# Optimization experiments

Hardware: AMD Instinct MI355X
Metric: run time of the kernel (lower is better)

Reference implementation:

```python
import jax, jax.numpy as jnp
import numpy as np

N_NODES = 50000
N_EDGES = 800000
D_IN = 128
HIDDEN = 128
NUM_GRAPHS = 64
NUM_CLASSES = 6


def setup_inputs() -> dict:
    key = jax.random.key(0)
    ks = jax.random.split(key, 12)
    x = jax.random.normal(ks[0], (N_NODES, D_IN), dtype=jnp.float32)
    edge_index = jax.random.randint(ks[1], (2, N_EDGES), 0, N_NODES, dtype=jnp.int64)
    batch = jnp.sort(jax.random.randint(ks[2], (N_NODES,), 0, NUM_GRAPHS, dtype=jnp.int64))
    def glorot(k, fan_in, fan_out):
        s = jnp.sqrt(6.0 / (fan_in + fan_out)).astype(jnp.float32)
        return jax.random.uniform(k, (fan_in, fan_out), jnp.float32, -s, s)
    W0 = glorot(ks[3], D_IN, HIDDEN)
    b0 = jnp.zeros((HIDDEN,), jnp.float32)
    W1 = glorot(ks[4], HIDDEN, HIDDEN)
    b1 = jnp.zeros((HIDDEN,), jnp.float32)
    W2 = glorot(ks[5], HIDDEN, HIDDEN)
    b2 = jnp.zeros((HIDDEN,), jnp.float32)
    lin_W = glorot(ks[6], HIDDEN, NUM_CLASSES)
    lin_b = jnp.zeros((NUM_CLASSES,), jnp.float32)
    return {"x": x, "edge_index": edge_index, "batch": batch,
            "W0": W0, "b0": b0, "W1": W1, "b1": b1, "W2": W2, "b2": b2,
            "lin_W": lin_W, "lin_b": lin_b}


def reference(x, edge_index, batch, W0, b0, W1, b1, W2, b2, lin_W, lin_b):
    # GCNConv (PyG default): add self-loops, symmetric degree norm,
    # out = scatter_add(norm * (xW)[src] -> dst) + bias, then ReLU.
    loop = jnp.arange(N_NODES, dtype=edge_index.dtype)
    src = jnp.concatenate([edge_index[0], loop])  # message sources (x_j)
    dst = jnp.concatenate([edge_index[1], loop])  # aggregation targets
    deg = jax.ops.segment_sum(jnp.ones_like(dst, x.dtype), dst, num_segments=N_NODES)
    dinv = jnp.where(deg > 0, jax.lax.rsqrt(deg), 0.0)
    norm = (dinv[src] * dinv[dst])[:, None]  # [E+N, 1]

    h = x
    for W, b in ((W0, b0), (W1, b1), (W2, b2)):
        hw = h @ W                                   # [N, H] dense projection
        agg = jax.ops.segment_sum(hw[src] * norm, dst, num_segments=N_NODES)
        h = jax.nn.relu(agg + b)

    # global_mean_pool over graph ids
    counts = jax.ops.segment_sum(jnp.ones((N_NODES,), x.dtype), batch, num_segments=NUM_GRAPHS)
    embedding = jax.ops.segment_sum(h, batch, num_segments=NUM_GRAPHS) / jnp.maximum(counts, 1.0)[:, None]
    # dropout is identity in eval mode
    logits = embedding @ lin_W + lin_b
    return logits, embedding
```

## Files before the change

### kernel.cpp

```cpp
#include <hip/hip_runtime.h>

#define N_NODES 50000
#define HIDDEN 128
#define NUM_GRAPHS 64
#define NUM_CLASSES 6
#define SLOT_SHIFT 6
#define NB 392
#define BUCKET_CAP 3072
#define P1_CHUNK 2048
#define CONV_BLOCKS 96
#define LSTR 136

typedef __attribute__((ext_vector_type(8))) short short8;
typedef __attribute__((ext_vector_type(4))) float float4v;
typedef __attribute__((ext_vector_type(2))) float float2v;

__device__ __forceinline__ unsigned short f2b(float f) {
    unsigned u = __float_as_uint(f);
    return (unsigned short)((u + 0x7FFFu + ((u >> 16) & 1u)) >> 16);
}
__device__ __forceinline__ unsigned char f2e4m3(float f) {
    return (unsigned char)(__builtin_amdgcn_cvt_pk_fp8_f32(f, f, 0, false) & 0xFF);
}

__global__ __launch_bounds__(512) void pass1(const float* __restrict__ W0, const float* __restrict__ W1,
                                             const float* __restrict__ W2, unsigned short* __restrict__ wb,
                                             const int* __restrict__ src, const int* __restrict__ dst,
                                             int* __restrict__ gcursor, unsigned* __restrict__ ebuf, int e) {
    if (blockIdx.x < CONV_BLOCKS) {
        int i = blockIdx.x * 512 + threadIdx.x;
        int wsel = i >> 14;
        int r = i & 16383;
        int j = r & 7;
        int lane = (r >> 3) & 63;
        int f = r >> 9;
        int ki = f >> 3, nt = f & 7;
        int k = ki * 32 + (lane >> 4) * 8 + j;
        int c = nt * 16 + (lane & 15);
        const float* W = (wsel == 0) ? W0 : ((wsel == 1) ? W1 : W2);
        wb[i] = f2b(W[k * 128 + c]);
        return;
    }
    __shared__ unsigned hist[NB];
    __shared__ unsigned base[NB];
    const int t = threadIdx.x;
    const int start = (blockIdx.x - CONV_BLOCKS) * P1_CHUNK;
    for (int i = t; i < NB; i += 512) hist[i] = 0;
    __syncthreads();
    int lb[4];
    unsigned pk[4], lr[4];
#pragma unroll
    for (int k = 0; k < 4; k++) {
        int i = start + k * 512 + t;
        lb[k] = -1;
        if (i < e) {
            int d = dst[i];
            int s = src[i];
            lb[k] = d >> 7;
            pk[k] = ((unsigned)(d & 127) << 16) | (unsigned)s;
            lr[k] = atomicAdd(&hist[lb[k]], 1u);
        }
    }
    __syncthreads();
    for (int b = t; b < NB; b += 512)
        base[b] = (unsigned)atomicAdd(&gcursor[b], (int)hist[b]);
    __syncthreads();
#pragma unroll
    for (int k = 0; k < 4; k++) {
        if (lb[k] >= 0) {
            unsigned pos = base[lb[k]] + lr[k];
            if (pos < BUCKET_CAP) ebuf[lb[k] * BUCKET_CAP + pos] = pk[k];
        }
    }
}

__global__ __launch_bounds__(512) void pass2(const unsigned* __restrict__ ebuf, const int* __restrict__ gcursor,
                                             const float* __restrict__ x,
                                             unsigned short* __restrict__ csr16, int* __restrict__ cntc,
                                             float* __restrict__ dinv, unsigned char* __restrict__ xs8, int n) {
    __shared__ unsigned short csr_lds[128 * 64];
    __shared__ unsigned cnt[128];
    const int b = blockIdx.x;
    const int t = threadIdx.x;
    if (t < 128) {
        cnt[t] = 0;
        csr_lds[t * 64] = (unsigned short)(b * 128 + t);
    }
    __syncthreads();
    const int nb = min(gcursor[b], BUCKET_CAP);
    for (int i = t; i < nb; i += 512) {
        unsigned e = ebuf[b * BUCKET_CAP + i];
        int dl = (int)(e >> 16);
        unsigned r = atomicAdd(&cnt[dl], 1u);
        if (r < 63) csr_lds[dl * 64 + 1 + r] = (unsigned short)(e & 0xFFFFu);
    }
    __syncthreads();
    {
        const unsigned* cu = (const unsigned*)csr_lds;
        unsigned* gout = (unsigned*)(csr16 + (size_t)b * 8192);
#pragma unroll
        for (int it = 0; it < 8; it++) gout[it * 512 + t] = cu[it * 512 + t];
    }
    if (t < 128) {
        int node = b * 128 + t;
        if (node < n) {
            int deg1 = (int)cnt[t] + 1;
            cntc[node] = min(deg1, 64);
            dinv[node] = rsqrtf((float)deg1);
        }
    }
#pragma unroll
    for (int it = 0; it < 8; it++) {
        int idx = it * 512 + t;
        int nl = idx >> 5;
        int el = (idx & 31) * 4;
        int gnode = b * 128 + nl;
        if (gnode < n) {
            float sc = rsqrtf((float)((int)cnt[nl] + 1));
            float4 v = *(const float4*)&x[gnode * 128 + el];
            unsigned lo = __builtin_amdgcn_cvt_pk_fp8_f32(v.x * sc, v.y * sc, 0, false);
            unsigned pkd = __builtin_amdgcn_cvt_pk_fp8_f32(v.z * sc, v.w * sc, lo, true);
            *(unsigned*)&xs8[gnode * 128 + el] = pkd;
        }
    }
}

__global__ __launch_bounds__(256) void fused_layer(const unsigned char* __restrict__ hs8,
                                                   const int* __restrict__ cntc,
                                                   const unsigned short* __restrict__ csr16,
                                                   const float* __restrict__ dinv,
                                                   const unsigned short* __restrict__ wb,
                                                   const float* __restrict__ bias,
                                                   const float* __restrict__ rowscale,
                                                   unsigned char* __restrict__ hout8,
                                                   const int* __restrict__ batchp,
                                                   float* __restrict__ embp) {
    __shared__ __align__(16) unsigned short tlds[16 * LSTR];
    __shared__ int bsh[16];
    const int wave = threadIdx.x >> 6;
    const int lane = threadIdx.x & 63;
    const int grp = lane >> 4;
    const int fl = lane & 15;
    const int node0 = blockIdx.x * 16;
    const int base_node = node0 + wave * 4;

    int nbv[4], mycv[4];
#pragma unroll
    for (int i = 0; i < 4; i++) nbv[i] = cntc[base_node + i];
#pragma unroll
    for (int i = 0; i < 4; i++)
        mycv[i] = (lane < nbv[i]) ? (int)csr16[((base_node + i) << SLOT_SHIFT) + lane] : 0;

    for (int i = 0; i < 4; i++) {
        const int node = base_node + i;
        const int nb = nbv[i];
        const int nbm1 = nb - 1;
        const int myc = mycv[i];
        float2v a01 = {0.f, 0.f}, a23 = {0.f, 0.f}, a45 = {0.f, 0.f}, a67 = {0.f, 0.f};

        const int nfull = nb >> 4;
        for (int h = 0; h < nfull; h++) {
            const int base = h << 4;
            int cc[4];
#pragma unroll
            for (int k = 0; k < 4; k++) cc[k] = __shfl(myc, base + k * 4 + grp, 64);
            uint2 u[4];
#pragma unroll
            for (int k = 0; k < 4; k++) u[k] = *(const uint2*)&hs8[cc[k] * 128 + fl * 8];
#pragma unroll
            for (int k = 0; k < 4; k++) {
                a01 += __builtin_amdgcn_cvt_pk_f32_fp8(u[k].x, false);
                a23 += __builtin_amdgcn_cvt_pk_f32_fp8(u[k].x, true);
                a45 += __builtin_amdgcn_cvt_pk_f32_fp8(u[k].y, false);
                a67 += __builtin_amdgcn_cvt_pk_f32_fp8(u[k].y, true);
            }
        }
        if (nb & 15) {
            const int base = nfull << 4;
            int cc[4];
            float mm[4];
#pragma unroll
            for (int k = 0; k < 4; k++) {
                int e = base + k * 4 + grp;
                mm[k] = (e < nb) ? 1.f : 0.f;
                cc[k] = __shfl(myc, min(e, nbm1), 64);
            }
            uint2 u[4];
#pragma unroll
            for (int k = 0; k < 4; k++) u[k] = *(const uint2*)&hs8[cc[k] * 128 + fl * 8];
#pragma unroll
            for (int k = 0; k < 4; k++) {
                float2v m2 = {mm[k], mm[k]};
                a01 += m2 * __builtin_amdgcn_cvt_pk_f32_fp8(u[k].x, false);
                a23 += m2 * __builtin_amdgcn_cvt_pk_f32_fp8(u[k].x, true);
                a45 += m2 * __builtin_amdgcn_cvt_pk_f32_fp8(u[k].y, false);
                a67 += m2 * __builtin_amdgcn_cvt_pk_f32_fp8(u[k].y, true);
            }
        }

        float acc[8] = {a01.x, a01.y, a23.x, a23.y, a45.x, a45.y, a67.x, a67.y};
#pragma unroll
        for (int j = 0; j < 8; j++) {
            acc[j] += __shfl_xor(acc[j], 16, 64);
            acc[j] += __shfl_xor(acc[j], 32, 64);
        }
        if (grp == 0) {
            const float dv = dinv[node];
            short8 o;
#pragma unroll
            for (int j = 0; j < 8; j++) o[j] = (short)f2b(acc[j] * dv);
            *(short8*)&tlds[(wave * 4 + i) * LSTR + fl * 8] = o;
        }
    }
    if (embp && threadIdx.x < 16) bsh[threadIdx.x] = batchp[node0 + threadIdx.x];
    __syncthreads();

    const int m = fl;
    const int quad = grp;
    const int nt0 = wave * 2;
    const short* B = (const short*)wb;
    float4v acc2[2];
    acc2[0] = (float4v){0.f, 0.f, 0.f, 0.f};
    acc2[1] = (float4v){0.f, 0.f, 0.f, 0.f};
#pragma unroll
    for (int ki = 0; ki < 4; ki++) {
        short8 a = *(const short8*)&tlds[m * LSTR + ki * 32 + quad * 8];
#pragma unroll
        for (int q = 0; q < 2; q++) {
            short8 b = *(const short8*)&B[((ki * 8 + nt0 + q) * 64 + lane) * 8];
            acc2[q] = __builtin_amdgcn_mfma_f32_16x16x32_bf16(a, b, acc2[q], 0, 0, 0);
        }
    }

    if (!embp) {
        float sc[4];
#pragma unroll
        for (int reg = 0; reg < 4; reg++) {
            int row = node0 + quad * 4 + reg;
            sc[reg] = rowscale[row];
        }
#pragma unroll
        for (int q = 0; q < 2; q++) {
            int c = (nt0 + q) * 16 + m;
            float bv = bias[c];
#pragma unroll
            for (int reg = 0; reg < 4; reg++) {
                int row = node0 + quad * 4 + reg;
                float v = fmaxf(acc2[q][reg] + bv, 0.f) * sc[reg];
                hout8[row * 128 + c] = f2e4m3(v);
            }
        }
    } else {
        const int g0 = bsh[0], g15 = bsh[15];
#pragma unroll
        for (int q = 0; q < 2; q++) {
            int c = (nt0 + q) * 16 + m;
            float bv = bias[c];
            float v0 = fmaxf(acc2[q][0] + bv, 0.f);
            float v1 = fmaxf(acc2[q][1] + bv, 0.f);
            float v2 = fmaxf(acc2[q][2] + bv, 0.f);
            float v3 = fmaxf(acc2[q][3] + bv, 0.f);
            if (g0 == g15) {
                float s = v0 + v1 + v2 + v3;
                s += __shfl_xor(s, 16, 64);
                s += __shfl_xor(s, 32, 64);
                if (quad == 0) atomicAdd(&embp[g0 * HIDDEN + c], s);
            } else {
                for (int gg = g0; gg <= g15; ++gg) {
                    float s = (bsh[quad * 4 + 0] == gg ? v0 : 0.f)
                            + (bsh[quad * 4 + 1] == gg ? v1 : 0.f)
                            + (bsh[quad * 4 + 2] == gg ? v2 : 0.f)
                            + (bsh[quad * 4 + 3] == gg ? v3 : 0.f);
                    s += __shfl_xor(s, 16, 64);
                    s += __shfl_xor(s, 32, 64);
                    if (quad == 0) atomicAdd(&embp[gg * HIDDEN + c], s);
                }
            }
        }
    }
}

__global__ __launch_bounds__(128) void finalize_kernel(const float* __restrict__ emb,
                                                       const int* __restrict__ batch,
                                                       const float* __restrict__ linW, const float* __restrict__ linb,
                                                       float* out, int n) {
    const int g = blockIdx.x;
    const int f = threadIdx.x;
    __shared__ float es[128];
    __shared__ int bnd[2];
    if (f < 2) {
        int target = g + f;
        int lo = 0, hi = n;
        while (lo < hi) {
            int mid = (lo + hi) >> 1;
            if (batch[mid] < target) lo = mid + 1; else hi = mid;
        }
        bnd[f] = lo;
    }
    __syncthreads();
    float c = (float)max(bnd[1] - bnd[0], 1);
    float e = emb[g * HIDDEN + f] / c;
    out[NUM_GRAPHS * NUM_CLASSES + g * HIDDEN + f] = e;
    es[f] = e;
    __syncthreads();
    if (f < NUM_CLASSES) {
        float s = linb[f];
        for (int k = 0; k < HIDDEN; k++) s += es[k] * linW[k * NUM_CLASSES + f];
        out[g * NUM_CLASSES + f] = s;
    }
}

extern "C" void kernel_launch(void* const* d_in, const int* in_sizes, int n_in,
                              void* d_out, int out_size, void* d_ws, size_t ws_size,
                              hipStream_t stream) {
    const float* x    = (const float*)d_in[0];
    const int*   ei   = (const int*)d_in[1];
    const int*   batch= (const int*)d_in[2];
    const float* W0   = (const float*)d_in[3];
    const float* b0   = (const float*)d_in[4];
    const float* W1   = (const float*)d_in[5];
    const float* b1   = (const float*)d_in[6];
    const float* W2   = (const float*)d_in[7];
    const float* b2   = (const float*)d_in[8];
    const float* linW = (const float*)d_in[9];
    const float* linb = (const float*)d_in[10];
    float* out = (float*)d_out;

    const int N = N_NODES;
    const int E = in_sizes[1] / 2;
    const int* srcp = ei;
    const int* dstp = ei + E;

    char* w = (char*)d_ws;
    size_t o = 0;
    auto alloc = [&](size_t bytes) { size_t r = o; o += (bytes + 255) & ~(size_t)255; return r; };
    int*            gcursor = (int*)           (w + alloc((size_t)NB * 4));
    float*          emb     = (float*)         (w + alloc((size_t)NUM_GRAPHS * HIDDEN * 4));
    size_t zero_bytes = o;
    unsigned*       ebuf    = (unsigned*)      (w + alloc((size_t)NB * BUCKET_CAP * 4));
    unsigned short* csr16   = (unsigned short*)(w + alloc((size_t)NB * 128 * 64 * 2));
    int*            cntc    = (int*)           (w + alloc((size_t)N * 4));
    float*          dinv    = (float*)         (w + alloc((size_t)N * 4));
    unsigned char*  xs8     = (unsigned char*) (w + alloc((size_t)(NB * 128) * HIDDEN));
    unsigned char*  h8a     = (unsigned char*) (w + alloc((size_t)(NB * 128) * HIDDEN));
    unsigned char*  h8b     = (unsigned char*) (w + alloc((size_t)(NB * 128) * HIDDEN));
    unsigned short* wb      = (unsigned short*)(w + alloc((size_t)3 * 16384 * 2));

    hipMemsetAsync(d_ws, 0, zero_bytes, stream);

    const int p1_edge_blocks = (E + P1_CHUNK - 1) / P1_CHUNK;

    pass1<<<CONV_BLOCKS + p1_edge_blocks, 512, 0, stream>>>(W0, W1, W2, wb, srcp, dstp, gcursor, ebuf, E);
    pass2<<<NB, 512, 0, stream>>>(ebuf, gcursor, x, csr16, cntc, dinv, xs8, N);

    const int fuse_grid = N / 16;

    fused_layer<<<fuse_grid, 256, 0, stream>>>(xs8, cntc, csr16, dinv, wb + 0 * 16384, b0, dinv, h8a, nullptr, nullptr);
    fused_layer<<<fuse_grid, 256, 0, stream>>>(h8a, cntc, csr16, dinv, wb + 1 * 16384, b1, dinv, h8b, nullptr, nullptr);
    fused_layer<<<fuse_grid, 256, 0, stream>>>(h8b, cntc, csr16, dinv, wb + 2 * 16384, b2, nullptr, nullptr, batch, emb);

    finalize_kernel<<<NUM_GRAPHS, 128, 0, stream>>>(emb, batch, linW, linb, out, N);
}
```

Baseline: 209.5 us.

## Use 64-node buckets, zero-row padded gathers, and fuse finalize into last layer

Edge buckets are halved to 64 destination nodes each (782 buckets) so the pass2 LDS footprint shrinks and more blocks run. Empty CSR slots now point to a zeroed padding row, so the aggregation loop handles groups of four edges without masks or per-lane neighbour-count checks. The separate finalize kernel is removed: the last-layer launch uses an atomic done-counter, and whichever block finishes last computes mean pooling and the linear head. This saves one launch but serialises the finalize work onto a single block and adds extra padding-row gathers.

```diff
diff --git a/kernel.cpp b/kernel.cpp
--- a/kernel.cpp
+++ b/kernel.cpp
@@ -5,8 +5,10 @@
 #define NUM_GRAPHS 64
 #define NUM_CLASSES 6
 #define SLOT_SHIFT 6
-#define NB 392
-#define BUCKET_CAP 3072
+#define NB 782
+#define NPAD 50048
+#define ZROW 50040
+#define BUCKET_CAP 1536
 #define P1_CHUNK 2048
 #define CONV_BLOCKS 96
 #define LSTR 136
@@ -56,8 +58,8 @@
         if (i < e) {
             int d = dst[i];
             int s = src[i];
-            lb[k] = d >> 7;
-            pk[k] = ((unsigned)(d & 127) << 16) | (unsigned)s;
+            lb[k] = d >> 6;
+            pk[k] = ((unsigned)(d & 63) << 16) | (unsigned)s;
             lr[k] = atomicAdd(&hist[lb[k]], 1u);
         }
     }
@@ -77,15 +79,22 @@
 __global__ __launch_bounds__(512) void pass2(const unsigned* __restrict__ ebuf, const int* __restrict__ gcursor,
                                              const float* __restrict__ x,
                                              unsigned short* __restrict__ csr16, int* __restrict__ cntc,
-                                             float* __restrict__ dinv, unsigned char* __restrict__ xs8, int n) {
-    __shared__ unsigned short csr_lds[128 * 64];
-    __shared__ unsigned cnt[128];
+                                             float* __restrict__ dinv, unsigned char* __restrict__ xs8,
+                                             unsigned char* __restrict__ h8a, unsigned char* __restrict__ h8b,
+                                             int n) {
+    __shared__ unsigned short csr_lds[64 * 64];
+    __shared__ unsigned cnt[64];
     const int b = blockIdx.x;
     const int t = threadIdx.x;
-    if (t < 128) {
-        cnt[t] = 0;
-        csr_lds[t * 64] = (unsigned short)(b * 128 + t);
-    }
+    {
+        const unsigned zz = ((unsigned)ZROW) | (((unsigned)ZROW) << 16);
+        unsigned* cl = (unsigned*)csr_lds;
+#pragma unroll
+        for (int it = 0; it < 4; it++) cl[it * 512 + t] = zz;
+    }
+    if (t < 64) cnt[t] = 0;
+    __syncthreads();
+    if (t < 64) csr_lds[t * 64] = (unsigned short)(b * 64 + t);
     __syncthreads();
     const int nb = min(gcursor[b], BUCKET_CAP);
     for (int i = t; i < nb; i += 512) {
@@ -97,12 +106,12 @@
     __syncthreads();
     {
         const unsigned* cu = (const unsigned*)csr_lds;
-        unsigned* gout = (unsigned*)(csr16 + (size_t)b * 8192);
-#pragma unroll
-        for (int it = 0; it < 8; it++) gout[it * 512 + t] = cu[it * 512 + t];
-    }
-    if (t < 128) {
-        int node = b * 128 + t;
+        unsigned* gout = (unsigned*)(csr16 + (size_t)b * 4096);
+#pragma unroll
+        for (int it = 0; it < 4; it++) gout[it * 512 + t] = cu[it * 512 + t];
+    }
+    if (t < 64) {
+        int node = b * 64 + t;
         if (node < n) {
             int deg1 = (int)cnt[t] + 1;
             cntc[node] = min(deg1, 64);
@@ -110,11 +119,11 @@
         }
     }
 #pragma unroll
-    for (int it = 0; it < 8; it++) {
+    for (int it = 0; it < 4; it++) {
         int idx = it * 512 + t;
         int nl = idx >> 5;
         int el = (idx & 31) * 4;
-        int gnode = b * 128 + nl;
+        int gnode = b * 64 + nl;
         if (gnode < n) {
             float sc = rsqrtf((float)((int)cnt[nl] + 1));
             float4 v = *(const float4*)&x[gnode * 128 + el];
@@ -123,20 +132,33 @@
             *(unsigned*)&xs8[gnode * 128 + el] = pkd;
         }
     }
-}
-
+    if (b == 0 && t < 384) {
+        uint4 z = {0, 0, 0, 0};
+        ((uint4*)(xs8 + (size_t)N_NODES * 128))[t] = z;
+        ((uint4*)(h8a + (size_t)N_NODES * 128))[t] = z;
+        ((uint4*)(h8b + (size_t)N_NODES * 128))[t] = z;
+    }
+}
+
+template <bool LAST>
 __global__ __launch_bounds__(256) void fused_layer(const unsigned char* __restrict__ hs8,
                                                    const int* __restrict__ cntc,
                                                    const unsigned short* __restrict__ csr16,
                                                    const float* __restrict__ dinv,
                                                    const unsigned short* __restrict__ wb,
                                                    const float* __restrict__ bias,
-                                                   const float* __restrict__ rowscale,
                                                    unsigned char* __restrict__ hout8,
                                                    const int* __restrict__ batchp,
-                                                   float* __restrict__ embp) {
+                                                   float* __restrict__ embp,
+                                                   const float* __restrict__ linW,
+                                                   const float* __restrict__ linb,
+                                                   float* __restrict__ out,
+                                                   unsigned* __restrict__ donep,
+                                                   int n) {
     __shared__ __align__(16) unsigned short tlds[16 * LSTR];
     __shared__ int bsh[16];
+    __shared__ int bnds[65];
+    __shared__ unsigned lastf;
     const int wave = threadIdx.x >> 6;
     const int lane = threadIdx.x & 63;
     const int grp = lane >> 4;
@@ -149,21 +171,19 @@
     for (int i = 0; i < 4; i++) nbv[i] = cntc[base_node + i];
 #pragma unroll
     for (int i = 0; i < 4; i++)
-        mycv[i] = (lane < nbv[i]) ? (int)csr16[((base_node + i) << SLOT_SHIFT) + lane] : 0;
+        mycv[i] = (int)csr16[((base_node + i) << SLOT_SHIFT) + lane];
 
     for (int i = 0; i < 4; i++) {
         const int node = base_node + i;
-        const int nb = nbv[i];
-        const int nbm1 = nb - 1;
+        const int nq = (nbv[i] + 3) >> 2;
         const int myc = mycv[i];
         float2v a01 = {0.f, 0.f}, a23 = {0.f, 0.f}, a45 = {0.f, 0.f}, a67 = {0.f, 0.f};
 
-        const int nfull = nb >> 4;
-        for (int h = 0; h < nfull; h++) {
-            const int base = h << 4;
+        int q = 0;
+        for (; q + 4 <= nq; q += 4) {
             int cc[4];
 #pragma unroll
-            for (int k = 0; k < 4; k++) cc[k] = __shfl(myc, base + k * 4 + grp, 64);
+            for (int k = 0; k < 4; k++) cc[k] = __shfl(myc, (q + k) * 4 + grp, 64);
             uint2 u[4];
 #pragma unroll
             for (int k = 0; k < 4; k++) u[k] = *(const uint2*)&hs8[cc[k] * 128 + fl * 8];
@@ -175,27 +195,29 @@
                 a67 += __builtin_amdgcn_cvt_pk_f32_fp8(u[k].y, true);
             }
         }
-        if (nb & 15) {
-            const int base = nfull << 4;
-            int cc[4];
-            float mm[4];
-#pragma unroll
-            for (int k = 0; k < 4; k++) {
-                int e = base + k * 4 + grp;
-                mm[k] = (e < nb) ? 1.f : 0.f;
-                cc[k] = __shfl(myc, min(e, nbm1), 64);
-            }
-            uint2 u[4];
-#pragma unroll
-            for (int k = 0; k < 4; k++) u[k] = *(const uint2*)&hs8[cc[k] * 128 + fl * 8];
-#pragma unroll
-            for (int k = 0; k < 4; k++) {
-                float2v m2 = {mm[k], mm[k]};
-                a01 += m2 * __builtin_amdgcn_cvt_pk_f32_fp8(u[k].x, false);
-                a23 += m2 * __builtin_amdgcn_cvt_pk_f32_fp8(u[k].x, true);
-                a45 += m2 * __builtin_amdgcn_cvt_pk_f32_fp8(u[k].y, false);
-                a67 += m2 * __builtin_amdgcn_cvt_pk_f32_fp8(u[k].y, true);
-            }
+        const int rem = nq - q;
+        int c0 = 0, c1 = 0, c2 = 0;
+        uint2 u0, u1, u2;
+        if (rem > 0) { c0 = __shfl(myc, (q + 0) * 4 + grp, 64); u0 = *(const uint2*)&hs8[c0 * 128 + fl * 8]; }
+        if (rem > 1) { c1 = __shfl(myc, (q + 1) * 4 + grp, 64); u1 = *(const uint2*)&hs8[c1 * 128 + fl * 8]; }
+        if (rem > 2) { c2 = __shfl(myc, (q + 2) * 4 + grp, 64); u2 = *(const uint2*)&hs8[c2 * 128 + fl * 8]; }
+        if (rem > 0) {
+            a01 += __builtin_amdgcn_cvt_pk_f32_fp8(u0.x, false);
+            a23 += __builtin_amdgcn_cvt_pk_f32_fp8(u0.x, true);
+            a45 += __builtin_amdgcn_cvt_pk_f32_fp8(u0.y, false);
+            a67 += __builtin_amdgcn_cvt_pk_f32_fp8(u0.y, true);
+        }
+        if (rem > 1) {
+            a01 += __builtin_amdgcn_cvt_pk_f32_fp8(u1.x, false);
+            a23 += __builtin_amdgcn_cvt_pk_f32_fp8(u1.x, true);
+            a45 += __builtin_amdgcn_cvt_pk_f32_fp8(u1.y, false);
+            a67 += __builtin_amdgcn_cvt_pk_f32_fp8(u1.y, true);
+        }
+        if (rem > 2) {
+            a01 += __builtin_amdgcn_cvt_pk_f32_fp8(u2.x, false);
+            a23 += __builtin_amdgcn_cvt_pk_f32_fp8(u2.x, true);
+            a45 += __builtin_amdgcn_cvt_pk_f32_fp8(u2.y, false);
+            a67 += __builtin_amdgcn_cvt_pk_f32_fp8(u2.y, true);
         }
 
         float acc[8] = {a01.x, a01.y, a23.x, a23.y, a45.x, a45.y, a67.x, a67.y};
@@ -212,7 +234,7 @@
             *(short8*)&tlds[(wave * 4 + i) * LSTR + fl * 8] = o;
         }
     }
-    if (embp && threadIdx.x < 16) bsh[threadIdx.x] = batchp[node0 + threadIdx.x];
+    if (LAST && threadIdx.x < 16) bsh[threadIdx.x] = batchp[node0 + threadIdx.x];
     __syncthreads();
 
     const int m = fl;
@@ -232,13 +254,10 @@
         }
     }
 
-    if (!embp) {
+    if (!LAST) {
         float sc[4];
 #pragma unroll
-        for (int reg = 0; reg < 4; reg++) {
-            int row = node0 + quad * 4 + reg;
-            sc[reg] = rowscale[row];
-        }
+        for (int reg = 0; reg < 4; reg++) sc[reg] = dinv[node0 + quad * 4 + reg];
 #pragma unroll
         for (int q = 0; q < 2; q++) {
             int c = (nt0 + q) * 16 + m;
@@ -277,36 +296,55 @@
                 }
             }
         }
-    }
-}
-
-__global__ __launch_bounds__(128) void finalize_kernel(const float* __restrict__ emb,
-                                                       const int* __restrict__ batch,
-                                                       const float* __restrict__ linW, const float* __restrict__ linb,
-                                                       float* out, int n) {
-    const int g = blockIdx.x;
-    const int f = threadIdx.x;
-    __shared__ float es[128];
-    __shared__ int bnd[2];
-    if (f < 2) {
-        int target = g + f;
-        int lo = 0, hi = n;
-        while (lo < hi) {
-            int mid = (lo + hi) >> 1;
-            if (batch[mid] < target) lo = mid + 1; else hi = mid;
-        }
-        bnd[f] = lo;
-    }
-    __syncthreads();
-    float c = (float)max(bnd[1] - bnd[0], 1);
-    float e = emb[g * HIDDEN + f] / c;
-    out[NUM_GRAPHS * NUM_CLASSES + g * HIDDEN + f] = e;
-    es[f] = e;
-    __syncthreads();
-    if (f < NUM_CLASSES) {
-        float s = linb[f];
-        for (int k = 0; k < HIDDEN; k++) s += es[k] * linW[k * NUM_CLASSES + f];
-        out[g * NUM_CLASSES + f] = s;
+
+        __syncthreads();
+        if (threadIdx.x == 0) {
+            __threadfence();
+            unsigned old = atomicAdd(donep, 1u);
+            lastf = (old == gridDim.x - 1) ? 1u : 0u;
+        }
+        __syncthreads();
+        if (lastf) {
+            const int t = threadIdx.x;
+            if (t < 65) {
+                int lo = 0, hi = n;
+                while (lo < hi) {
+                    int mid = (lo + hi) >> 1;
+                    if (batchp[mid] < t) lo = mid + 1; else hi = mid;
+                }
+                bnds[t] = lo;
+            }
+            __syncthreads();
+            const int g = t >> 2;
+            const int part = t & 3;
+            float cgr = (float)max(bnds[g + 1] - bnds[g], 1);
+            float s0 = 0.f, s1 = 0.f, s2 = 0.f, s3 = 0.f, s4 = 0.f, s5 = 0.f;
+            for (int f0 = 0; f0 < 32; f0++) {
+                int f = part * 32 + f0;
+                float e = atomicAdd(&embp[g * HIDDEN + f], 0.0f) / cgr;
+                out[NUM_GRAPHS * NUM_CLASSES + g * HIDDEN + f] = e;
+                s0 += e * linW[f * NUM_CLASSES + 0];
+                s1 += e * linW[f * NUM_CLASSES + 1];
+                s2 += e * linW[f * NUM_CLASSES + 2];
+                s3 += e * linW[f * NUM_CLASSES + 3];
+                s4 += e * linW[f * NUM_CLASSES + 4];
+                s5 += e * linW[f * NUM_CLASSES + 5];
+            }
+#pragma unroll
+            for (int d = 1; d <= 2; d <<= 1) {
+                s0 += __shfl_xor(s0, d, 64); s1 += __shfl_xor(s1, d, 64);
+                s2 += __shfl_xor(s2, d, 64); s3 += __shfl_xor(s3, d, 64);
+                s4 += __shfl_xor(s4, d, 64); s5 += __shfl_xor(s5, d, 64);
+            }
+            if (part == 0) {
+                out[g * NUM_CLASSES + 0] = s0 + linb[0];
+                out[g * NUM_CLASSES + 1] = s1 + linb[1];
+                out[g * NUM_CLASSES + 2] = s2 + linb[2];
+                out[g * NUM_CLASSES + 3] = s3 + linb[3];
+                out[g * NUM_CLASSES + 4] = s4 + linb[4];
+                out[g * NUM_CLASSES + 5] = s5 + linb[5];
+            }
+        }
     }
 }
 
@@ -336,14 +374,15 @@
     auto alloc = [&](size_t bytes) { size_t r = o; o += (bytes + 255) & ~(size_t)255; return r; };
     int*            gcursor = (int*)           (w + alloc((size_t)NB * 4));
     float*          emb     = (float*)         (w + alloc((size_t)NUM_GRAPHS * HIDDEN * 4));
+    unsigned*       done    = (unsigned*)      (w + alloc(256));
     size_t zero_bytes = o;
     unsigned*       ebuf    = (unsigned*)      (w + alloc((size_t)NB * BUCKET_CAP * 4));
-    unsigned short* csr16   = (unsigned short*)(w + alloc((size_t)NB * 128 * 64 * 2));
+    unsigned short* csr16   = (unsigned short*)(w + alloc((size_t)NB * 64 * 64 * 2));
     int*            cntc    = (int*)           (w + alloc((size_t)N * 4));
     float*          dinv    = (float*)         (w + alloc((size_t)N * 4));
-    unsigned char*  xs8     = (unsigned char*) (w + alloc((size_t)(NB * 128) * HIDDEN));
-    unsigned char*  h8a     = (unsigned char*) (w + alloc((size_t)(NB * 128) * HIDDEN));
-    unsigned char*  h8b     = (unsigned char*) (w + alloc((size_t)(NB * 128) * HIDDEN));
+    unsigned char*  xs8     = (unsigned char*) (w + alloc((size_t)NPAD * HIDDEN));
+    unsigned char*  h8a     = (unsigned char*) (w + alloc((size_t)NPAD * HIDDEN));
+    unsigned char*  h8b     = (unsigned char*) (w + alloc((size_t)NPAD * HIDDEN));
     unsigned short* wb      = (unsigned short*)(w + alloc((size_t)3 * 16384 * 2));
 
     hipMemsetAsync(d_ws, 0, zero_bytes, stream);
@@ -351,13 +390,14 @@
     const int p1_edge_blocks = (E + P1_CHUNK - 1) / P1_CHUNK;
 
     pass1<<<CONV_BLOCKS + p1_edge_blocks, 512, 0, stream>>>(W0, W1, W2, wb, srcp, dstp, gcursor, ebuf, E);
-    pass2<<<NB, 512, 0, stream>>>(ebuf, gcursor, x, csr16, cntc, dinv, xs8, N);
+    pass2<<<NB, 512, 0, stream>>>(ebuf, gcursor, x, csr16, cntc, dinv, xs8, h8a, h8b, N);
 
     const int fuse_grid = N / 16;
 
-    fused_layer<<<fuse_grid, 256, 0, stream>>>(xs8, cntc, csr16, dinv, wb + 0 * 16384, b0, dinv, h8a, nullptr, nullptr);
-    fused_layer<<<fuse_grid, 256, 0, stream>>>(h8a, cntc, csr16, dinv, wb + 1 * 16384, b1, dinv, h8b, nullptr, nullptr);
-    fused_layer<<<fuse_grid, 256, 0, stream>>>(h8b, cntc, csr16, dinv, wb + 2 * 16384, b2, nullptr, nullptr, batch, emb);
-
-    finalize_kernel<<<NUM_GRAPHS, 128, 0, stream>>>(emb, batch, linW, linb, out, N);
-}
+    fused_layer<false><<<fuse_grid, 256, 0, stream>>>(xs8, cntc, csr16, dinv, wb + 0 * 16384, b0, h8a,
+                                                      nullptr, nullptr, nullptr, nullptr, nullptr, nullptr, N);
+    fused_layer<false><<<fuse_grid, 256, 0, stream>>>(h8a, cntc, csr16, dinv, wb + 1 * 16384, b1, h8b,
+                                                      nullptr, nullptr, nullptr, nullptr, nullptr, nullptr, N);
+    fused_layer<true><<<fuse_grid, 256, 0, stream>>>(h8b, cntc, csr16, dinv, wb + 2 * 16384, b2, nullptr,
+                                                     batch, emb, linW, linb, out, done, N);
+}
```

New measurement: 282.5 us. +34.8%, slower.

## Pad CSR slots with zero-row index and halve bucket size to remove tail masking

Applied to the files above, without the earlier changes.

Destination buckets shrink from 128 to 64 nodes, so pass2 runs twice as many blocks (782), each with smaller LDS and bucket capacity. Unused CSR slots are filled with a sentinel index pointing at a zeroed padding row appended to each fp8 feature buffer. This lets the gather loop run whole groups of 16 with no masked tail iteration and no per-lane bounds check on CSR loads. The layer kernel is templated on last-layer mode to drop runtime branches. The cost is some wasted gathers of the zero row for partially filled groups, and the smaller bucket capacity raises the risk of overflow that would silently drop edges.

```diff
diff --git a/kernel.cpp b/kernel.cpp
--- a/kernel.cpp
+++ b/kernel.cpp
@@ -5,8 +5,10 @@
 #define NUM_GRAPHS 64
 #define NUM_CLASSES 6
 #define SLOT_SHIFT 6
-#define NB 392
-#define BUCKET_CAP 3072
+#define NB 782
+#define NPAD 50048
+#define ZROW 50040
+#define BUCKET_CAP 1536
 #define P1_CHUNK 2048
 #define CONV_BLOCKS 96
 #define LSTR 136
@@ -56,8 +58,8 @@
         if (i < e) {
             int d = dst[i];
             int s = src[i];
-            lb[k] = d >> 7;
-            pk[k] = ((unsigned)(d & 127) << 16) | (unsigned)s;
+            lb[k] = d >> 6;
+            pk[k] = ((unsigned)(d & 63) << 16) | (unsigned)s;
             lr[k] = atomicAdd(&hist[lb[k]], 1u);
         }
     }
@@ -77,15 +79,22 @@
 __global__ __launch_bounds__(512) void pass2(const unsigned* __restrict__ ebuf, const int* __restrict__ gcursor,
                                              const float* __restrict__ x,
                                              unsigned short* __restrict__ csr16, int* __restrict__ cntc,
-                                             float* __restrict__ dinv, unsigned char* __restrict__ xs8, int n) {
-    __shared__ unsigned short csr_lds[128 * 64];
-    __shared__ unsigned cnt[128];
+                                             float* __restrict__ dinv, unsigned char* __restrict__ xs8,
+                                             unsigned char* __restrict__ h8a, unsigned char* __restrict__ h8b,
+                                             int n) {
+    __shared__ unsigned short csr_lds[64 * 64];
+    __shared__ unsigned cnt[64];
     const int b = blockIdx.x;
     const int t = threadIdx.x;
-    if (t < 128) {
-        cnt[t] = 0;
-        csr_lds[t * 64] = (unsigned short)(b * 128 + t);
-    }
+    {
+        const unsigned zz = ((unsigned)ZROW) | (((unsigned)ZROW) << 16);
+        unsigned* cl = (unsigned*)csr_lds;
+#pragma unroll
+        for (int it = 0; it < 4; it++) cl[it * 512 + t] = zz;
+    }
+    if (t < 64) cnt[t] = 0;
+    __syncthreads();
+    if (t < 64) csr_lds[t * 64] = (unsigned short)(b * 64 + t);
     __syncthreads();
     const int nb = min(gcursor[b], BUCKET_CAP);
     for (int i = t; i < nb; i += 512) {
@@ -97,12 +106,12 @@
     __syncthreads();
     {
         const unsigned* cu = (const unsigned*)csr_lds;
-        unsigned* gout = (unsigned*)(csr16 + (size_t)b * 8192);
-#pragma unroll
-        for (int it = 0; it < 8; it++) gout[it * 512 + t] = cu[it * 512 + t];
-    }
-    if (t < 128) {
-        int node = b * 128 + t;
+        unsigned* gout = (unsigned*)(csr16 + (size_t)b * 4096);
+#pragma unroll
+        for (int it = 0; it < 4; it++) gout[it * 512 + t] = cu[it * 512 + t];
+    }
+    if (t < 64) {
+        int node = b * 64 + t;
         if (node < n) {
             int deg1 = (int)cnt[t] + 1;
             cntc[node] = min(deg1, 64);
@@ -110,11 +119,11 @@
         }
     }
 #pragma unroll
-    for (int it = 0; it < 8; it++) {
+    for (int it = 0; it < 4; it++) {
         int idx = it * 512 + t;
         int nl = idx >> 5;
         int el = (idx & 31) * 4;
-        int gnode = b * 128 + nl;
+        int gnode = b * 64 + nl;
         if (gnode < n) {
             float sc = rsqrtf((float)((int)cnt[nl] + 1));
             float4 v = *(const float4*)&x[gnode * 128 + el];
@@ -123,15 +132,21 @@
             *(unsigned*)&xs8[gnode * 128 + el] = pkd;
         }
     }
-}
-
+    if (b == 0 && t < 384) {
+        uint4 z = {0, 0, 0, 0};
+        ((uint4*)(xs8 + (size_t)N_NODES * 128))[t] = z;
+        ((uint4*)(h8a + (size_t)N_NODES * 128))[t] = z;
+        ((uint4*)(h8b + (size_t)N_NODES * 128))[t] = z;
+    }
+}
+
+template <bool LAST>
 __global__ __launch_bounds__(256) void fused_layer(const unsigned char* __restrict__ hs8,
                                                    const int* __restrict__ cntc,
                                                    const unsigned short* __restrict__ csr16,
                                                    const float* __restrict__ dinv,
                                                    const unsigned short* __restrict__ wb,
                                                    const float* __restrict__ bias,
-                                                   const float* __restrict__ rowscale,
                                                    unsigned char* __restrict__ hout8,
                                                    const int* __restrict__ batchp,
                                                    float* __restrict__ embp) {
@@ -149,18 +164,16 @@
     for (int i = 0; i < 4; i++) nbv[i] = cntc[base_node + i];
 #pragma unroll
     for (int i = 0; i < 4; i++)
-        mycv[i] = (lane < nbv[i]) ? (int)csr16[((base_node + i) << SLOT_SHIFT) + lane] : 0;
+        mycv[i] = (int)csr16[((base_node + i) << SLOT_SHIFT) + lane];
 
     for (int i = 0; i < 4; i++) {
         const int node = base_node + i;
-        const int nb = nbv[i];
-        const int nbm1 = nb - 1;
+        const int ng = (nbv[i] + 15) >> 4;
         const int myc = mycv[i];
         float2v a01 = {0.f, 0.f}, a23 = {0.f, 0.f}, a45 = {0.f, 0.f}, a67 = {0.f, 0.f};
 
-        const int nfull = nb >> 4;
-        for (int h = 0; h < nfull; h++) {
-            const int base = h << 4;
+        for (int g4 = 0; g4 < ng; g4++) {
+            const int base = g4 << 4;
             int cc[4];
 #pragma unroll
             for (int k = 0; k < 4; k++) cc[k] = __shfl(myc, base + k * 4 + grp, 64);
@@ -175,28 +188,6 @@
                 a67 += __builtin_amdgcn_cvt_pk_f32_fp8(u[k].y, true);
             }
         }
-        if (nb & 15) {
-            const int base = nfull << 4;
-            int cc[4];
-            float mm[4];
-#pragma unroll
-            for (int k = 0; k < 4; k++) {
-                int e = base + k * 4 + grp;
-                mm[k] = (e < nb) ? 1.f : 0.f;
-                cc[k] = __shfl(myc, min(e, nbm1), 64);
-            }
-            uint2 u[4];
-#pragma unroll
-            for (int k = 0; k < 4; k++) u[k] = *(const uint2*)&hs8[cc[k] * 128 + fl * 8];
-#pragma unroll
-            for (int k = 0; k < 4; k++) {
-                float2v m2 = {mm[k], mm[k]};
-                a01 += m2 * __builtin_amdgcn_cvt_pk_f32_fp8(u[k].x, false);
-                a23 += m2 * __builtin_amdgcn_cvt_pk_f32_fp8(u[k].x, true);
-                a45 += m2 * __builtin_amdgcn_cvt_pk_f32_fp8(u[k].y, false);
-                a67 += m2 * __builtin_amdgcn_cvt_pk_f32_fp8(u[k].y, true);
-            }
-        }
 
         float acc[8] = {a01.x, a01.y, a23.x, a23.y, a45.x, a45.y, a67.x, a67.y};
 #pragma unroll
@@ -212,7 +203,7 @@
             *(short8*)&tlds[(wave * 4 + i) * LSTR + fl * 8] = o;
         }
     }
-    if (embp && threadIdx.x < 16) bsh[threadIdx.x] = batchp[node0 + threadIdx.x];
+    if (LAST && threadIdx.x < 16) bsh[threadIdx.x] = batchp[node0 + threadIdx.x];
     __syncthreads();
 
     const int m = fl;
@@ -232,13 +223,10 @@
         }
     }
 
-    if (!embp) {
+    if (!LAST) {
         float sc[4];
 #pragma unroll
-        for (int reg = 0; reg < 4; reg++) {
-            int row = node0 + quad * 4 + reg;
-            sc[reg] = rowscale[row];
-        }
+        for (int reg = 0; reg < 4; reg++) sc[reg] = dinv[node0 + quad * 4 + reg];
 #pragma unroll
         for (int q = 0; q < 2; q++) {
             int c = (nt0 + q) * 16 + m;
@@ -338,12 +326,12 @@
     float*          emb     = (float*)         (w + alloc((size_t)NUM_GRAPHS * HIDDEN * 4));
     size_t zero_bytes = o;
     unsigned*       ebuf    = (unsigned*)      (w + alloc((size_t)NB * BUCKET_CAP * 4));
-    unsigned short* csr16   = (unsigned short*)(w + alloc((size_t)NB * 128 * 64 * 2));
+    unsigned short* csr16   = (unsigned short*)(w + alloc((size_t)NB * 64 * 64 * 2));
     int*            cntc    = (int*)           (w + alloc((size_t)N * 4));
     float*          dinv    = (float*)         (w + alloc((size_t)N * 4));
-    unsigned char*  xs8     = (unsigned char*) (w + alloc((size_t)(NB * 128) * HIDDEN));
-    unsigned char*  h8a     = (unsigned char*) (w + alloc((size_t)(NB * 128) * HIDDEN));
-    unsigned char*  h8b     = (unsigned char*) (w + alloc((size_t)(NB * 128) * HIDDEN));
+    unsigned char*  xs8     = (unsigned char*) (w + alloc((size_t)NPAD * HIDDEN));
+    unsigned char*  h8a     = (unsigned char*) (w + alloc((size_t)NPAD * HIDDEN));
+    unsigned char*  h8b     = (unsigned char*) (w + alloc((size_t)NPAD * HIDDEN));
     unsigned short* wb      = (unsigned short*)(w + alloc((size_t)3 * 16384 * 2));
 
     hipMemsetAsync(d_ws, 0, zero_bytes, stream);
@@ -351,13 +339,16 @@
     const int p1_edge_blocks = (E + P1_CHUNK - 1) / P1_CHUNK;
 
     pass1<<<CONV_BLOCKS + p1_edge_blocks, 512, 0, stream>>>(W0, W1, W2, wb, srcp, dstp, gcursor, ebuf, E);
-    pass2<<<NB, 512, 0, stream>>>(ebuf, gcursor, x, csr16, cntc, dinv, xs8, N);
+    pass2<<<NB, 512, 0, stream>>>(ebuf, gcursor, x, csr16, cntc, dinv, xs8, h8a, h8b, N);
 
     const int fuse_grid = N / 16;
 
-    fused_layer<<<fuse_grid, 256, 0, stream>>>(xs8, cntc, csr16, dinv, wb + 0 * 16384, b0, dinv, h8a, nullptr, nullptr);
-    fused_layer<<<fuse_grid, 256, 0, stream>>>(h8a, cntc, csr16, dinv, wb + 1 * 16384, b1, dinv, h8b, nullptr, nullptr);
-    fused_layer<<<fuse_grid, 256, 0, stream>>>(h8b, cntc, csr16, dinv, wb + 2 * 16384, b2, nullptr, nullptr, batch, emb);
+    fused_layer<false><<<fuse_grid, 256, 0, stream>>>(xs8, cntc, csr16, dinv, wb + 0 * 16384, b0, h8a,
+                                                      nullptr, nullptr);
+    fused_layer<false><<<fuse_grid, 256, 0, stream>>>(h8a, cntc, csr16, dinv, wb + 1 * 16384, b1, h8b,
+                                                      nullptr, nullptr);
+    fused_layer<true><<<fuse_grid, 256, 0, stream>>>(h8b, cntc, csr16, dinv, wb + 2 * 16384, b2, nullptr,
+                                                     batch, emb);
 
     finalize_kernel<<<NUM_GRAPHS, 128, 0, stream>>>(emb, batch, linW, linb, out, N);
 }
```

Measured after the change: 196.9 us. 1.06x faster.
